# Kernel tuning notes

Hardware: AMD Instinct MI355X
Metric: run time of the kernel (lower is better)

Reference implementation:

```python
import jax, jax.numpy as jnp
import numpy as np

RADIUS = 3
DIAM = 2 * RADIUS + 1  # 7
NP = DIAM * DIAM       # 49 taps


def _cubic(d, a=-0.75):
    # torch bicubic kernel (a = -0.75)
    d = np.abs(d)
    return np.where(d <= 1, (a + 2) * d**3 - (a + 3) * d**2 + 1,
                    np.where(d < 2, a * d**3 - 5 * a * d**2 + 8 * a * d - 4 * a, 0.0))


def _resize_matrix(out_size, in_size):
    # dense [out,in] matrix reproducing torch F.interpolate bicubic, align_corners=False
    i = np.arange(out_size)
    x = (i + 0.5) * in_size / out_size - 0.5
    x0 = np.floor(x).astype(np.int64)
    t = x - x0
    W = np.zeros((out_size, in_size), np.float32)
    for k in range(-1, 3):
        w = _cubic(t - k)
        idx = np.clip(x0 + k, 0, in_size - 1)  # border replicate
        np.add.at(W, (i, idx), w.astype(np.float32))
    return jnp.asarray(W)


def _bicubic(x, GH, GW):
    B, C, H, W = x.shape
    Wh = _resize_matrix(GH, H)
    Ww = _resize_matrix(GW, W)
    return jnp.einsum('Hh,bchw,Ww->bcHW', Wh, x, Ww)


def _jbu(source, guidance, w1, b1, w2, b2, temp, sigma):
    # FeatUp JBULearnedRange.forward (eval mode: Dropout2d is identity)
    B, _, GH, GW = guidance.shape
    # range_proj: 1x1 conv -> GELU -> 1x1 conv
    q = jnp.einsum('kc,bchw->bkhw', w1, guidance) + b1[None, :, None, None]
    q = jax.nn.gelu(q, approximate=False)
    q = jnp.einsum('kc,bchw->bkhw', w2, q) + b2[None, :, None, None]  # [B,32,GH,GW]
    qp = jnp.pad(q, ((0, 0), (0, 0), (RADIUS, RADIUS), (RADIUS, RADIUS)), mode='reflect')
    # scores[b,p,h,w] = <key at center, key at offset p> (avoids B*32*49*H*W unfold)
    scores = jnp.stack([jnp.sum(qp[:, :, di:di + GH, dj:dj + GW] * q, axis=1)
                        for di in range(DIAM) for dj in range(DIAM)], axis=1)  # [B,49,GH,GW]
    t = jnp.clip(jnp.exp(temp), 1e-4, 1e4)
    range_kernel = jax.nn.softmax(t * scores, axis=1)
    dist = jnp.linspace(-1.0, 1.0, DIAM)
    gy, gx = jnp.meshgrid(dist, dist, indexing='ij')
    spatial_kernel = jnp.exp(-(gy**2 + gx**2) / (2.0 * sigma**2)).reshape(1, NP, 1, 1)
    k = range_kernel * spatial_kernel
    k = k / jnp.clip(jnp.sum(k, axis=1, keepdims=True), 1e-7, None)
    hr = _bicubic(source, GH, GW)
    hrp = jnp.pad(hr, ((0, 0), (0, 0), (RADIUS, RADIUS), (RADIUS, RADIUS)), mode='reflect')
    # AdaptiveConv: per-pixel 7x7 kernel applied to all channels
    out = jnp.zeros_like(hr)
    p_idx = 0
    for di in range(DIAM):
        for dj in range(DIAM):
            out = out + hrp[:, :, di:di + GH, dj:dj + GW] * k[:, p_idx][:, None]
            p_idx += 1
    return out


def _forward(x, guidance, linear_w, linear_b, w1s, b1s, w2s, b2s, temps, sigmas):
    f = (x @ linear_w.T + linear_b).reshape(-1, 3, 18, 18)
    for i in range(4):  # up1..up4, each fed the FULL guidance as in the Decoder
        f = _jbu(f, guidance, w1s[i], b1s[i], w2s[i], b2s[i], temps[i], sigmas[i])
    return f


def setup_inputs() -> dict:
    key = jax.random.key(0)
    ks = jax.random.split(key, 6)
    B = 8
    return {
        'x': jax.random.normal(ks[0], (B, 1000), jnp.float32),
        'guidance': jax.random.uniform(ks[1], (B, 3, 224, 224), jnp.float32),
        'linear_w': jax.random.normal(ks[2], (972, 1000), jnp.float32) * 0.03,
        'linear_b': jnp.zeros((972,), jnp.float32),
        'w1s': jax.random.normal(ks[3], (4, 32, 3), jnp.float32) * 0.1,
        'b1s': jnp.zeros((4, 32), jnp.float32),
        'w2s': jax.random.normal(ks[4], (4, 32, 32), jnp.float32) * 0.1,
        'b2s': jnp.zeros((4, 32), jnp.float32),
        'temps': jnp.zeros((4,), jnp.float32),   # range_temp init 0.0
        'sigmas': jnp.ones((4,), jnp.float32),   # sigma_spatial init 1.0
    }


def reference(x, guidance, linear_w, linear_b, w1s, b1s, w2s, b2s, temps, sigmas):
    return _forward(x, guidance, linear_w, linear_b, w1s, b1s, w2s, b2s, temps, sigmas)
```

## Files before the change

kernel.cpp:

```cpp
#include <hip/hip_runtime.h>
#include <hip/hip_fp16.h>
#include <math.h>

#define GHH 224
#define GWW 224
#define HW (GHH*GWW)
#define BATCH 8
#define RAD 3
#define DIAM 7
#define QC 32
#define TILE 16
#define TP (TILE + 2*RAD)
#define TPIX (TP*TP)
#define CS 485

#define HRH_COLS 24
#define PSTR (TP*HRH_COLS)
#define HRH_B (8*PSTR*2)
#define SMEM_B (HRH_B + 4*CS*16)

#define L2E 1.44269504f

typedef _Float16 h2 __attribute__((ext_vector_type(2)));
typedef _Float16 v8h __attribute__((ext_vector_type(8)));
typedef float v4f __attribute__((ext_vector_type(4)));

__device__ __forceinline__ int refl(int i) {
    if (i < 0) i = -i;
    if (i >= GHH) i = 2 * GHH - 2 - i;
    return i;
}

__device__ __forceinline__ float gelu_fast(float v) {
    float u = 0.7978845608f * v * (1.f + 0.044715f * v * v);
    float e = __builtin_amdgcn_exp2f(u * (2.f * L2E));
    float th = 1.f - 2.f / (e + 1.f);
    return 0.5f * v * (1.f + th);
}

__global__ void linear_prep_kernel(const float* __restrict__ x,
                                   const float* __restrict__ W,
                                   const float* __restrict__ bias,
                                   float* __restrict__ f0,
                                   const float* __restrict__ w2s,
                                   __half* __restrict__ wsB,
                                   const float* __restrict__ w1s,
                                   const float* __restrict__ b1s,
                                   __half* __restrict__ wsW1,
                                   const float* __restrict__ guid,
                                   float4* __restrict__ guid4) {
    int blk = blockIdx.x;
    if (blk >= 1946) {
        int i = (blk - 1946) * 256 + threadIdx.x;
        int b = i / HW, pix = i % HW;
        guid4[i] = make_float4(guid[(b * 3) * HW + pix],
                               guid[(b * 3 + 1) * HW + pix],
                               guid[(b * 3 + 2) * HW + pix], 0.f);
        return;
    }
    if (blk == 1945) {
        int tid = threadIdx.x;
        if (tid < 128) {
            int s = tid >> 5, c = tid & 31;
            wsW1[tid * 4 + 0] = __float2half(w1s[s * 96 + c * 3 + 0]);
            wsW1[tid * 4 + 1] = __float2half(w1s[s * 96 + c * 3 + 1]);
            wsW1[tid * 4 + 2] = __float2half(w1s[s * 96 + c * 3 + 2]);
            wsW1[tid * 4 + 3] = __float2half(b1s[s * 32 + c]);
        }
        return;
    }
    if (blk == 1944) {
        int tid = threadIdx.x;
        int s = tid >> 6, l = tid & 63;
        int n0 = l & 15, kq = l >> 4;
        const float* w2 = w2s + s * 1024;
        __half* dst = wsB + (size_t)tid * 16;
        #pragma unroll
        for (int j = 0; j < 8; j++) {
            dst[j]     = __float2half(w2[n0 * QC + kq * 8 + j]);
            dst[8 + j] = __float2half(w2[(n0 + 16) * QC + kq * 8 + j]);
        }
        return;
    }
    int gwave = (blk * blockDim.x + threadIdx.x) >> 6;
    int lane = threadIdx.x & 63;
    if (gwave >= BATCH * 972) return;
    int b = gwave / 972, j = gwave % 972;
    const float* xr = x + b * 1000;
    const float* wr = W + j * 1000;
    float s = 0.f;
    for (int k = lane; k < 1000; k += 64)
        s += xr[k] * wr[k];
    #pragma unroll
    for (int off = 32; off; off >>= 1) s += __shfl_down(s, off, 64);
    if (lane == 0) f0[gwave] = s + bias[j];
}

__device__ __forceinline__ float cubicw(float d) {
    d = fabsf(d);
    if (d <= 1.f) return ((1.25f * d - 2.25f) * d) * d + 1.f;
    if (d < 2.f)  return ((-0.75f * d + 3.75f) * d - 6.f) * d + 3.f;
    return 0.f;
}

__global__ void bicubic_kernel(const float* __restrict__ f0, float4* __restrict__ hr4) {
    int idx = blockIdx.x * blockDim.x + threadIdx.x;
    if (idx >= BATCH * HW) return;
    int pix = idx % HW;
    int b = idx / HW;
    int w = pix % GWW, h = pix / GWW;
    float xx = (w + 0.5f) * (18.f / 224.f) - 0.5f;
    float yy = (h + 0.5f) * (18.f / 224.f) - 0.5f;
    float fx0 = floorf(xx), fy0 = floorf(yy);
    int x0 = (int)fx0, y0 = (int)fy0;
    float tx = xx - fx0, ty = yy - fy0;
    float wx[4], wy[4];
    int ix[4], iy[4];
    #pragma unroll
    for (int k = 0; k < 4; k++) {
        wx[k] = cubicw(tx - (float)(k - 1));
        wy[k] = cubicw(ty - (float)(k - 1));
        int a = x0 + (k - 1); ix[k] = min(max(a, 0), 17);
        a = y0 + (k - 1);     iy[k] = min(max(a, 0), 17);
    }
    float acc[3];
    #pragma unroll
    for (int c = 0; c < 3; c++) {
        const float* src = f0 + (b * 3 + c) * 324;
        float a = 0.f;
        #pragma unroll
        for (int ky = 0; ky < 4; ky++) {
            float rowv = 0.f;
            #pragma unroll
            for (int kx = 0; kx < 4; kx++) rowv += wx[kx] * src[iy[ky] * 18 + ix[kx]];
            a += wy[ky] * rowv;
        }
        acc[c] = a;
    }
    hr4[idx] = make_float4(acc[0], acc[1], acc[2], 0.f);
}

__global__ __launch_bounds__(256) void q_kernel(
    const float4* __restrict__ guid4,
    const __half* __restrict__ wsW1,
    const __half* __restrict__ wsB, const float* __restrict__ b2,
    float4* __restrict__ qimg,
    int stage)
{
    const int tid = threadIdx.x;
    const int l = tid & 63;
    const int gw = (blockIdx.x * 256 + tid) >> 6;
    const int n0 = l & 15, kq = l >> 4;
    const int b = gw / 392;
    const int pix0 = (gw - b * 392) * 128;

    const v8h* Bp = (const v8h*)(wsB + ((size_t)stage * 64 + l) * 16);
    const v8h W2a = Bp[0], W2b = Bp[1];
    const float4 b2a = *(const float4*)(b2 + 4 * kq);
    const float4 b2b = *(const float4*)(b2 + 16 + 4 * kq);
    union { _Float16 h[32]; float4 f4[4]; } W1;
    {
        const float4* wp = (const float4*)(wsW1 + stage * 128 + kq * 32);
        W1.f4[0] = wp[0]; W1.f4[1] = wp[1]; W1.f4[2] = wp[2]; W1.f4[3] = wp[3];
    }
    const int plane0 = kq >> 1;
    const int boff   = (kq & 1) * 8;
    char* qc = (char*)qimg;

    #pragma unroll 1
    for (int it = 0; it < 8; it++) {
        int pix = pix0 + it * 16 + n0;
        float4 g = guid4[(size_t)b * HW + pix];
        union { _Float16 h[8]; v8h v; } A;
        #pragma unroll
        for (int j = 0; j < 8; j++) {
            float vv = fmaf((float)W1.h[j * 4], g.x,
                       fmaf((float)W1.h[j * 4 + 1], g.y,
                       fmaf((float)W1.h[j * 4 + 2], g.z, (float)W1.h[j * 4 + 3])));
            A.h[j] = (_Float16)gelu_fast(vv);
        }
        v4f D0 = {0.f, 0.f, 0.f, 0.f}, D1 = {0.f, 0.f, 0.f, 0.f};
        D0 = __builtin_amdgcn_mfma_f32_16x16x32_f16(W2a, A.v, D0, 0, 0, 0);
        D1 = __builtin_amdgcn_mfma_f32_16x16x32_f16(W2b, A.v, D1, 0, 0, 0);
        union { _Float16 h[4]; uint2 u; } q0, q1;
        q0.h[0] = (_Float16)(D0[0] + b2a.x);
        q0.h[1] = (_Float16)(D0[1] + b2a.y);
        q0.h[2] = (_Float16)(D0[2] + b2a.z);
        q0.h[3] = (_Float16)(D0[3] + b2a.w);
        q1.h[0] = (_Float16)(D1[0] + b2b.x);
        q1.h[1] = (_Float16)(D1[1] + b2b.y);
        q1.h[2] = (_Float16)(D1[2] + b2b.z);
        q1.h[3] = (_Float16)(D1[3] + b2b.w);
        *(uint2*)(qc + ((size_t)(b * 4 + plane0) * HW + pix) * 16 + boff)     = q0.u;
        *(uint2*)(qc + ((size_t)(b * 4 + 2 + plane0) * HW + pix) * 16 + boff) = q1.u;
    }
}

__global__ __launch_bounds__(256, 4) void jbu_kernel(
    const float4* __restrict__ qimg,
    const float4* __restrict__ hr4,
    float4* __restrict__ out4,
    float* __restrict__ outP,
    const float* __restrict__ temps,
    const float* __restrict__ sigmas,
    int stage)
{
    __shared__ __align__(16) char smem[SMEM_B];
    _Float16* hrh = (_Float16*)smem;
    char* sqb = smem + HRH_B;
    float4* sqf4 = (float4*)sqb;

    const int tx = threadIdx.x, ty = threadIdx.y;
    const int tid = ty * TILE + tx;
    const int b = blockIdx.z;
    const int h0 = blockIdx.y * TILE, w0 = blockIdx.x * TILE;

    const float4* qb = qimg + (size_t)b * 4 * HW;
    const float4* hb = hr4 + (size_t)b * HW;
    for (int i = tid; i < TPIX; i += 256) {
        int r = i / TP, cx = i % TP;
        int gh = refl(h0 - RAD + r), gw = refl(w0 - RAD + cx);
        size_t gpix = (size_t)gh * GWW + gw;
        sqf4[i]          = qb[gpix];
        sqf4[CS + i]     = qb[HW + gpix];
        sqf4[2 * CS + i] = qb[2 * HW + gpix];
        sqf4[3 * CS + i] = qb[3 * HW + gpix];
        float4 v = hb[gpix];
        _Float16 hx = (_Float16)v.x, hy = (_Float16)v.y, hz = (_Float16)v.z;
        int base = r * HRH_COLS + cx;
        hrh[0 * PSTR + base] = hx;
        hrh[1 * PSTR + base] = hy;
        hrh[2 * PSTR + base] = hz;
        hrh[3 * PSTR + base] = (_Float16)1.0f;
        hrh[4 * PSTR + base] = (_Float16)(v.x - (float)hx);
        hrh[5 * PSTR + base] = (_Float16)(v.y - (float)hy);
        hrh[6 * PSTR + base] = (_Float16)(v.z - (float)hz);
        hrh[7 * PSTR + base] = (_Float16)0.0f;
    }
    for (int i = tid; i < 8 * TP * 2; i += 256) {
        int p = i / (TP * 2), rem = i % (TP * 2);
        int r = rem >> 1, cc = 22 + (rem & 1);
        hrh[p * PSTR + r * HRH_COLS + cc] = (_Float16)0.0f;
    }
    __syncthreads();

    const int wv = tid >> 6;
    const int l = tid & 63;
    const int g = l >> 4, c = l & 15;

    float t = __expf(temps[stage]);
    t = fminf(fmaxf(t, 1e-4f), 1e4f);
    const float tl2 = t * L2E;
    float sig = sigmas[stage];
    float inv2s2 = 1.f / (2.f * sig * sig);
    float sdv[DIAM];
    #pragma unroll
    for (int i = 0; i < DIAM; i++) {
        float d = (float)(i - 3) * (1.f / 3.f);
        sdv[i] = __expf(-d * d * inv2s2);
    }
    float lc2[8];
    #pragma unroll
    for (int jj = 0; jj < 8; jj++) {
        int dj = 8 * g + jj - c;
        float d = (float)(dj - 3) * (1.f / 3.f);
        lc2[jj] = (dj >= 0 && dj <= 6) ? (-d * d * inv2s2 * L2E) : -1.44e38f;
    }
    const int nbb = 8 * (c >> 2) + (c & 3);
    const int nb0 = min(nbb, 21);
    const int nb1 = min(nbb + 4, 21);
    const int pA = c & 3;

    #pragma unroll 1
    for (int rr = 0; rr < 4; rr++) {
        const int row = wv * 4 + rr;
        const v8h Bc = *(const v8h*)(sqb + (size_t)(g * CS + (row + RAD) * TP + RAD + c) * 16);
        v4f D2 = {0.f, 0.f, 0.f, 0.f};
        #pragma unroll
        for (int di = 0; di < DIAM; di++) {
            const int prow = row + di;
            const v8h A0 = *(const v8h*)(sqb + (size_t)(g * CS + prow * TP + nb0) * 16);
            const v8h A1 = *(const v8h*)(sqb + (size_t)(g * CS + prow * TP + nb1) * 16);
            v4f S0 = {0.f, 0.f, 0.f, 0.f}, S1 = {0.f, 0.f, 0.f, 0.f};
            S0 = __builtin_amdgcn_mfma_f32_16x16x32_f16(A0, Bc, S0, 0, 0, 0);
            S1 = __builtin_amdgcn_mfma_f32_16x16x32_f16(A1, Bc, S1, 0, 0, 0);
            const float sy = sdv[di];
            union { _Float16 h[8]; v8h v; } Wg;
            #pragma unroll
            for (int j = 0; j < 4; j++) {
                Wg.h[j]     = (_Float16)(__builtin_amdgcn_exp2f(fmaf(S0[j], tl2, lc2[j])) * sy);
                Wg.h[4 + j] = (_Float16)(__builtin_amdgcn_exp2f(fmaf(S1[j], tl2, lc2[4 + j])) * sy);
            }
            const v8h Hh = *(const v8h*)(smem + (size_t)((pA * TP + prow) * HRH_COLS + 8 * g) * 2);
            const v8h Hl = *(const v8h*)(smem + (size_t)(((pA + 4) * TP + prow) * HRH_COLS + 8 * g) * 2);
            D2 = __builtin_amdgcn_mfma_f32_16x16x32_f16(Hh, Wg.v, D2, 0, 0, 0);
            D2 = __builtin_amdgcn_mfma_f32_16x16x32_f16(Hl, Wg.v, D2, 0, 0, 0);
        }
        if (l < 16) {
            float rk = 1.f / fmaxf(D2[3], 1e-7f);
            if (stage < 3) {
                out4[(size_t)b * HW + (size_t)(h0 + row) * GWW + (w0 + c)] =
                    make_float4(D2[0] * rk, D2[1] * rk, D2[2] * rk, 0.f);
            } else {
                size_t obase = (size_t)b * 3 * HW + (size_t)(h0 + row) * GWW + (w0 + c);
                outP[obase]          = D2[0] * rk;
                outP[obase + HW]     = D2[1] * rk;
                outP[obase + 2 * HW] = D2[2] * rk;
            }
        }
    }
}

extern "C" void kernel_launch(void* const* d_in, const int* in_sizes, int n_in,
                              void* d_out, int out_size, void* d_ws, size_t ws_size,
                              hipStream_t stream) {
    const float* x      = (const float*)d_in[0];
    const float* guid   = (const float*)d_in[1];
    const float* lw     = (const float*)d_in[2];
    const float* lb     = (const float*)d_in[3];
    const float* w1s    = (const float*)d_in[4];
    const float* b1s    = (const float*)d_in[5];
    const float* w2s    = (const float*)d_in[6];
    const float* b2s    = (const float*)d_in[7];
    const float* temps  = (const float*)d_in[8];
    const float* sigmas = (const float*)d_in[9];

    char* ws = (char*)d_ws;
    const size_t P4_BYTES = (size_t)BATCH * HW * sizeof(float4);
    float4* guid4 = (float4*)ws;
    float4* hr4A  = (float4*)(ws + P4_BYTES);
    float4* hr4B  = (float4*)(ws + 2 * P4_BYTES);
    float*  f0    = (float*)(ws + 3 * P4_BYTES);
    __half* wsB   = (__half*)(ws + 3 * P4_BYTES + 31104);
    __half* wsW1  = (__half*)(ws + 3 * P4_BYTES + 31104 + 8192);
    float4* qimg  = (float4*)(ws + 3 * P4_BYTES + 40320);

    linear_prep_kernel<<<1946 + 1568, 256, 0, stream>>>(
        x, lw, lb, f0, w2s, wsB, w1s, b1s, wsW1, guid, guid4);
    bicubic_kernel<<<(BATCH * HW + 255) / 256, 256, 0, stream>>>(f0, hr4A);

    dim3 jgrid(14, 14, BATCH), jblock(16, 16);
    const float4* hins[4]  = { hr4A, hr4B, hr4A, hr4B };
    float4*       fouts[4] = { hr4B, hr4A, hr4B, nullptr };
    for (int s = 0; s < 4; s++) {
        q_kernel<<<784, 256, 0, stream>>>(guid4, wsW1, wsB, b2s + s * 32, qimg, s);
        jbu_kernel<<<jgrid, jblock, 0, stream>>>(
            qimg, hins[s], fouts[s], (s == 3) ? (float*)d_out : nullptr,
            temps, sigmas, s);
    }
}
```

Before: 279.2 us.

## Fuse bicubic upsample into first JBU stage and read planar guidance directly

Removes the separate bicubic kernel by computing the bicubic-interpolated source on the fly while stage 0 of the JBU kernel loads its haloed tile. It also drops the guidance repacking into float4, so q_kernel reads the three planar guidance channels directly. This saves two passes over full-resolution buffers and one launch. In exchange, stage 0 recomputes bicubic values for halo pixels, and q_kernel issues three strided scalar loads instead of one vector load.

```diff
diff --git a/kernel.cpp b/kernel.cpp
--- a/kernel.cpp
+++ b/kernel.cpp
@@ -38,6 +38,45 @@
     return 0.5f * v * (1.f + th);
 }
 
+__device__ __forceinline__ float cubicw(float d) {
+    d = fabsf(d);
+    if (d <= 1.f) return ((1.25f * d - 2.25f) * d) * d + 1.f;
+    if (d < 2.f)  return ((-0.75f * d + 3.75f) * d - 6.f) * d + 3.f;
+    return 0.f;
+}
+
+__device__ __forceinline__ float4 bicubic_px(const float* __restrict__ f0, int b, int h, int w) {
+    float xx = (w + 0.5f) * (18.f / 224.f) - 0.5f;
+    float yy = (h + 0.5f) * (18.f / 224.f) - 0.5f;
+    float fx0 = floorf(xx), fy0 = floorf(yy);
+    int x0 = (int)fx0, y0 = (int)fy0;
+    float tx = xx - fx0, ty = yy - fy0;
+    float wx[4], wy[4];
+    int ix[4], iy[4];
+    #pragma unroll
+    for (int k = 0; k < 4; k++) {
+        wx[k] = cubicw(tx - (float)(k - 1));
+        wy[k] = cubicw(ty - (float)(k - 1));
+        int a = x0 + (k - 1); ix[k] = min(max(a, 0), 17);
+        a = y0 + (k - 1);     iy[k] = min(max(a, 0), 17);
+    }
+    float acc[3];
+    #pragma unroll
+    for (int c = 0; c < 3; c++) {
+        const float* src = f0 + (b * 3 + c) * 324;
+        float a = 0.f;
+        #pragma unroll
+        for (int ky = 0; ky < 4; ky++) {
+            float rowv = 0.f;
+            #pragma unroll
+            for (int kx = 0; kx < 4; kx++) rowv += wx[kx] * src[iy[ky] * 18 + ix[kx]];
+            a += wy[ky] * rowv;
+        }
+        acc[c] = a;
+    }
+    return make_float4(acc[0], acc[1], acc[2], 0.f);
+}
+
 __global__ void linear_prep_kernel(const float* __restrict__ x,
                                    const float* __restrict__ W,
                                    const float* __restrict__ bias,
@@ -46,18 +85,8 @@
                                    __half* __restrict__ wsB,
                                    const float* __restrict__ w1s,
                                    const float* __restrict__ b1s,
-                                   __half* __restrict__ wsW1,
-                                   const float* __restrict__ guid,
-                                   float4* __restrict__ guid4) {
+                                   __half* __restrict__ wsW1) {
     int blk = blockIdx.x;
-    if (blk >= 1946) {
-        int i = (blk - 1946) * 256 + threadIdx.x;
-        int b = i / HW, pix = i % HW;
-        guid4[i] = make_float4(guid[(b * 3) * HW + pix],
-                               guid[(b * 3 + 1) * HW + pix],
-                               guid[(b * 3 + 2) * HW + pix], 0.f);
-        return;
-    }
     if (blk == 1945) {
         int tid = threadIdx.x;
         if (tid < 128) {
@@ -96,52 +125,8 @@
     if (lane == 0) f0[gwave] = s + bias[j];
 }
 
-__device__ __forceinline__ float cubicw(float d) {
-    d = fabsf(d);
-    if (d <= 1.f) return ((1.25f * d - 2.25f) * d) * d + 1.f;
-    if (d < 2.f)  return ((-0.75f * d + 3.75f) * d - 6.f) * d + 3.f;
-    return 0.f;
-}
-
-__global__ void bicubic_kernel(const float* __restrict__ f0, float4* __restrict__ hr4) {
-    int idx = blockIdx.x * blockDim.x + threadIdx.x;
-    if (idx >= BATCH * HW) return;
-    int pix = idx % HW;
-    int b = idx / HW;
-    int w = pix % GWW, h = pix / GWW;
-    float xx = (w + 0.5f) * (18.f / 224.f) - 0.5f;
-    float yy = (h + 0.5f) * (18.f / 224.f) - 0.5f;
-    float fx0 = floorf(xx), fy0 = floorf(yy);
-    int x0 = (int)fx0, y0 = (int)fy0;
-    float tx = xx - fx0, ty = yy - fy0;
-    float wx[4], wy[4];
-    int ix[4], iy[4];
-    #pragma unroll
-    for (int k = 0; k < 4; k++) {
-        wx[k] = cubicw(tx - (float)(k - 1));
-        wy[k] = cubicw(ty - (float)(k - 1));
-        int a = x0 + (k - 1); ix[k] = min(max(a, 0), 17);
-        a = y0 + (k - 1);     iy[k] = min(max(a, 0), 17);
-    }
-    float acc[3];
-    #pragma unroll
-    for (int c = 0; c < 3; c++) {
-        const float* src = f0 + (b * 3 + c) * 324;
-        float a = 0.f;
-        #pragma unroll
-        for (int ky = 0; ky < 4; ky++) {
-            float rowv = 0.f;
-            #pragma unroll
-            for (int kx = 0; kx < 4; kx++) rowv += wx[kx] * src[iy[ky] * 18 + ix[kx]];
-            a += wy[ky] * rowv;
-        }
-        acc[c] = a;
-    }
-    hr4[idx] = make_float4(acc[0], acc[1], acc[2], 0.f);
-}
-
 __global__ __launch_bounds__(256) void q_kernel(
-    const float4* __restrict__ guid4,
+    const float* __restrict__ guid,
     const __half* __restrict__ wsW1,
     const __half* __restrict__ wsB, const float* __restrict__ b2,
     float4* __restrict__ qimg,
@@ -165,18 +150,21 @@
     }
     const int plane0 = kq >> 1;
     const int boff   = (kq & 1) * 8;
+    const float* gb = guid + (size_t)b * 3 * HW;
     char* qc = (char*)qimg;
 
     #pragma unroll 1
     for (int it = 0; it < 8; it++) {
         int pix = pix0 + it * 16 + n0;
-        float4 g = guid4[(size_t)b * HW + pix];
+        float gx = gb[pix];
+        float gy = gb[HW + pix];
+        float gz = gb[2 * HW + pix];
         union { _Float16 h[8]; v8h v; } A;
         #pragma unroll
         for (int j = 0; j < 8; j++) {
-            float vv = fmaf((float)W1.h[j * 4], g.x,
-                       fmaf((float)W1.h[j * 4 + 1], g.y,
-                       fmaf((float)W1.h[j * 4 + 2], g.z, (float)W1.h[j * 4 + 3])));
+            float vv = fmaf((float)W1.h[j * 4], gx,
+                       fmaf((float)W1.h[j * 4 + 1], gy,
+                       fmaf((float)W1.h[j * 4 + 2], gz, (float)W1.h[j * 4 + 3])));
             A.h[j] = (_Float16)gelu_fast(vv);
         }
         v4f D0 = {0.f, 0.f, 0.f, 0.f}, D1 = {0.f, 0.f, 0.f, 0.f};
@@ -199,6 +187,7 @@
 __global__ __launch_bounds__(256, 4) void jbu_kernel(
     const float4* __restrict__ qimg,
     const float4* __restrict__ hr4,
+    const float* __restrict__ f0,
     float4* __restrict__ out4,
     float* __restrict__ outP,
     const float* __restrict__ temps,
@@ -225,7 +214,9 @@
         sqf4[CS + i]     = qb[HW + gpix];
         sqf4[2 * CS + i] = qb[2 * HW + gpix];
         sqf4[3 * CS + i] = qb[3 * HW + gpix];
-        float4 v = hb[gpix];
+        float4 v;
+        if (stage == 0) v = bicubic_px(f0, b, gh, gw);
+        else            v = hb[gpix];
         _Float16 hx = (_Float16)v.x, hy = (_Float16)v.y, hz = (_Float16)v.z;
         int base = r * HRH_COLS + cx;
         hrh[0 * PSTR + base] = hx;
@@ -327,7 +318,6 @@
 
     char* ws = (char*)d_ws;
     const size_t P4_BYTES = (size_t)BATCH * HW * sizeof(float4);
-    float4* guid4 = (float4*)ws;
     float4* hr4A  = (float4*)(ws + P4_BYTES);
     float4* hr4B  = (float4*)(ws + 2 * P4_BYTES);
     float*  f0    = (float*)(ws + 3 * P4_BYTES);
@@ -335,17 +325,16 @@
     __half* wsW1  = (__half*)(ws + 3 * P4_BYTES + 31104 + 8192);
     float4* qimg  = (float4*)(ws + 3 * P4_BYTES + 40320);
 
-    linear_prep_kernel<<<1946 + 1568, 256, 0, stream>>>(
-        x, lw, lb, f0, w2s, wsB, w1s, b1s, wsW1, guid, guid4);
-    bicubic_kernel<<<(BATCH * HW + 255) / 256, 256, 0, stream>>>(f0, hr4A);
+    linear_prep_kernel<<<1946, 256, 0, stream>>>(
+        x, lw, lb, f0, w2s, wsB, w1s, b1s, wsW1);
 
     dim3 jgrid(14, 14, BATCH), jblock(16, 16);
     const float4* hins[4]  = { hr4A, hr4B, hr4A, hr4B };
     float4*       fouts[4] = { hr4B, hr4A, hr4B, nullptr };
     for (int s = 0; s < 4; s++) {
-        q_kernel<<<784, 256, 0, stream>>>(guid4, wsW1, wsB, b2s + s * 32, qimg, s);
+        q_kernel<<<784, 256, 0, stream>>>(guid, wsW1, wsB, b2s + s * 32, qimg, s);
         jbu_kernel<<<jgrid, jblock, 0, stream>>>(
-            qimg, hins[s], fouts[s], (s == 3) ? (float*)d_out : nullptr,
+            qimg, hins[s], f0, fouts[s], (s == 3) ? (float*)d_out : nullptr,
             temps, sigmas, s);
     }
 }
```

After: 284.2 us. About the same (+1.8%).
